# Performance work log

Hardware: AMD Instinct MI355X
Metric: run time of the kernel (lower is better)

Reference implementation:

```python
import jax, jax.numpy as jnp
import numpy as np

N_QUBITS = 8
N_LAYERS = 4


def _apply_1q(state, U, q):
    """Apply a 2x2 gate U (shape (2,2) shared, or (B,2,2) per-sample) on qubit q.
    state: (B, 2, 2, ..., 2) with qubit q on axis q+1 (wire 0 = most significant)."""
    a = q + 1
    st = jnp.moveaxis(state, a, -1)
    shp = st.shape
    st = st.reshape(shp[0], -1, 2)  # (B, rest, 2)
    if U.ndim == 3:
        st = jnp.einsum('bij,brj->bri', U, st)
    else:
        st = jnp.einsum('ij,brj->bri', U, st)
    return jnp.moveaxis(st.reshape(shp), -1, a)


def _cnot(state, c, t):
    ac, at = c + 1, t + 1
    s0 = jnp.take(state, 0, axis=ac)
    s1 = jnp.take(state, 1, axis=ac)
    at2 = at - 1 if at > ac else at  # axis shift after removing control axis
    s1 = jnp.flip(s1, axis=at2)      # X on target where control = 1
    return jnp.stack([s0, s1], axis=ac)


def _rx(t):
    c = jnp.cos(t / 2)
    s = jnp.sin(t / 2)
    return jnp.stack([jnp.stack([c + 0j, -1j * s]),
                      jnp.stack([-1j * s, c + 0j])]).astype(jnp.complex64)


def _ry(t):
    c = jnp.cos(t / 2)
    s = jnp.sin(t / 2)
    return jnp.stack([jnp.stack([c, -s]),
                      jnp.stack([s, c])]).astype(jnp.complex64)


def _rz(t):
    return jnp.diag(jnp.stack([jnp.exp(-1j * t / 2),
                               jnp.exp(1j * t / 2)])).astype(jnp.complex64)


def _ry_batched(t):
    # t: (B,) -> (B, 2, 2)
    c = jnp.cos(t / 2)
    s = jnp.sin(t / 2)
    U = jnp.stack([jnp.stack([c, -s], axis=-1),
                   jnp.stack([s, c], axis=-1)], axis=-2)
    return U.astype(jnp.complex64)


def setup_inputs() -> dict:
    key = jax.random.key(0)
    k1, k2 = jax.random.split(key)
    B = 16384
    x = jax.random.normal(k1, (B, N_QUBITS), dtype=jnp.float32)
    weights = jax.random.normal(k2, (N_QUBITS * N_LAYERS * 3,), dtype=jnp.float32) * 0.1
    return {"x": x, "weights": weights}


def reference(x, weights):
    n, L = N_QUBITS, N_LAYERS
    B = x.shape[0]
    state = jnp.zeros((B,) + (2,) * n, dtype=jnp.complex64)
    state = state.at[(slice(None),) + (0,) * n].set(1.0)

    # angle encoding: per-sample RY on each wire
    for q in range(n):
        state = _apply_1q(state, _ry_batched(x[:, q]), q)

    idx = 0
    for _ in range(L):
        for q in range(n):
            state = _apply_1q(state, _rx(weights[idx]), q)
            state = _apply_1q(state, _ry(weights[idx + 1]), q)
            state = _apply_1q(state, _rz(weights[idx + 2]), q)
            idx += 3
        for q in range(n - 1):
            state = _cnot(state, q, q + 1)

    p = jnp.abs(state) ** 2  # (B, 2, ..., 2) float32
    outs = []
    for q in range(n):
        axes = tuple(a for a in range(1, n + 1) if a != q + 1)
        z = p.sum(axis=axes)  # (B, 2)
        outs.append(z[:, 0] - z[:, 1])
    return jnp.stack(outs, axis=-1).astype(jnp.float32)
```

## Files before the change

kernel.cpp:

```cpp
#include <hip/hip_runtime.h>


#define NGATES 32

constexpr bool selon(int l, int d) {
    return (l == 0) ? (d == 0) : (((d + l - 1) & (l - 1)) == (l - 1));
}
constexpr int lm_of(int l, int q) {
    int m = 0;
    for (int d = 0; q + d <= 7; ++d)
        if ((l & d) == d) { int qq = q + d; if (qq <= 3) m |= 1 << (3 - qq); }
    return m;
}
constexpr int rm_of(int l, int q) {
    int m = 0;
    for (int d = 0; q + d <= 7; ++d)
        if ((l & d) == d) { int qq = q + d; if (qq >= 4) m |= 1 << (7 - qq); }
    return m;
}
constexpr int slm_of(int l, int q) {
    int m = 0;
    for (int d = 0; d <= q; ++d)
        if (selon(l, d)) { int k = q - d; if (k <= 3) m |= 1 << (3 - k); }
    return m;
}
constexpr int srm_of(int l, int q) {
    int m = 0;
    for (int d = 0; d <= q; ++d)
        if (selon(l, d)) { int k = q - d; if (k >= 4) m |= 1 << (7 - k); }
    return m;
}

__device__ __forceinline__ float xsgn(float f, unsigned m) {
    return __int_as_float(__float_as_int(f) ^ (int)m);
}

template<int M>
__device__ __forceinline__ float shx(float v) {
    return __int_as_float(__builtin_amdgcn_ds_swizzle(__float_as_int(v), (M << 10) | 0x1F));
}

template<int LM, int RM, int SLM, int SRM>
__device__ __forceinline__ void apply_gate(float ar[16], float ai[16], int lane,
                                           const float4 g)
{
    unsigned sm = 0;
    if constexpr (SLM != 0)
        sm = (unsigned)((__builtin_popcount(lane & SLM) & 1) << 31);
    const float c0r = g.x, c1i = g.w;
    const float c0i0 = xsgn(g.y, sm);
    const float c1r0 = xsgn(g.z, sm);
    const float c0i1 = xsgn(g.y, sm ^ 0x80000000u);
    const float c1r1 = xsgn(g.z, sm ^ 0x80000000u);

    if constexpr (RM == 0) {
        #pragma unroll
        for (int r = 0; r < 16; ++r) {
            const bool c1 = (__builtin_popcount(r & SRM) & 1) != 0;
            const float c0i = c1 ? c0i1 : c0i0;
            const float c1r = c1 ? c1r1 : c1r0;
            const float br = shx<LM>(ar[r]);
            const float bi = shx<LM>(ai[r]);
            const float nr = c0r*ar[r] - c0i*ai[r] + c1r*br - c1i*bi;
            const float ni = c0r*ai[r] + c0i*ar[r] + c1r*bi + c1i*br;
            ar[r] = nr; ai[r] = ni;
        }
    } else {
        #pragma unroll
        for (int r = 0; r < 16; ++r) {
            const int p = r ^ RM;
            if (p < r) continue;
            float br_r, bi_r, br_p, bi_p;
            if constexpr (LM != 0) {
                br_r = shx<LM>(ar[p]); bi_r = shx<LM>(ai[p]);
                br_p = shx<LM>(ar[r]); bi_p = shx<LM>(ai[r]);
            } else {
                br_r = ar[p]; bi_r = ai[p];
                br_p = ar[r]; bi_p = ai[r];
            }
            const bool cr = (__builtin_popcount(r & SRM) & 1) != 0;
            const bool cp = (__builtin_popcount(p & SRM) & 1) != 0;
            const float c0i_r = cr ? c0i1 : c0i0, c1r_r = cr ? c1r1 : c1r0;
            const float c0i_p = cp ? c0i1 : c0i0, c1r_p = cp ? c1r1 : c1r0;
            const float nr_r = c0r*ar[r] - c0i_r*ai[r] + c1r_r*br_r - c1i*bi_r;
            const float ni_r = c0r*ai[r] + c0i_r*ar[r] + c1r_r*bi_r + c1i*br_r;
            const float nr_p = c0r*ar[p] - c0i_p*ai[p] + c1r_p*br_p - c1i*bi_p;
            const float ni_p = c0r*ai[p] + c0i_p*ar[p] + c1r_p*bi_p + c1i*br_p;
            ar[r] = nr_r; ai[r] = ni_r;
            ar[p] = nr_p; ai[p] = ni_p;
        }
    }
}

#define GATE(L, Q) apply_gate<lm_of(L,Q), rm_of(L,Q), slm_of(L,Q), srm_of(L,Q)>( \
                       ar, ai, lane, gsh4[(L)*8+(Q)])
#define LAYER(L) GATE(L,0); GATE(L,1); GATE(L,2); GATE(L,3); \
                 GATE(L,4); GATE(L,5); GATE(L,6); GATE(L,7);

__global__ __launch_bounds__(256, 4) void qsim(const float* __restrict__ x,
                                               const float* __restrict__ w,
                                               float* __restrict__ out, int B)
{
    __shared__ float4 gsh4[NGATES];

    const int tid = threadIdx.x;
    if (tid < NGATES) {
        float hx = 0.5f * w[tid*3+0];
        float hy = 0.5f * w[tid*3+1];
        float hz = 0.5f * w[tid*3+2];
        float cx = cosf(hx), sx = sinf(hx);
        float cy = cosf(hy), sy = sinf(hy);
        float cz = cosf(hz), sz = sinf(hz);
        float m00r = cy*cx,  m00i =  sy*sx;
        float m01r = -sy*cx, m01i = -cy*sx;
        gsh4[tid] = make_float4(cz*m00r + sz*m00i,
                                cz*m00i - sz*m00r,
                                cz*m01r + sz*m01i,
                                cz*m01i - sz*m01r);
    }
    __syncthreads();

    const int lane = tid & 63;
    const int il   = lane & 15;
    const int sample = blockIdx.x * 16 + (tid >> 4);
    if (sample >= B) return;

    const float4* xp = (const float4*)(x + sample * 8);
    float4 xa = xp[0], xb = xp[1];
    float xs[8] = {xa.x, xa.y, xa.z, xa.w, xb.x, xb.y, xb.z, xb.w};
    float cq[8], sq[8];
    #pragma unroll
    for (int q = 0; q < 8; ++q) {
        float h = 0.5f * xs[q];
        __sincosf(h, &sq[q], &cq[q]);
    }
    float lp = ((il & 8) ? sq[0] : cq[0]);
    lp      *= ((il & 4) ? sq[1] : cq[1]);
    lp      *= ((il & 2) ? sq[2] : cq[2]);
    lp      *= ((il & 1) ? sq[3] : cq[3]);
    float t67[4] = {cq[6]*cq[7], cq[6]*sq[7], sq[6]*cq[7], sq[6]*sq[7]};
    float a5[2]  = {cq[5], sq[5]};
    float a4[2]  = {cq[4]*lp, sq[4]*lp};
    float ar[16], ai[16];
    #pragma unroll
    for (int r = 0; r < 16; ++r) {
        ar[r] = a4[(r >> 3) & 1] * a5[(r >> 2) & 1] * t67[r & 3];
        ai[r] = 0.f;
    }

    LAYER(0)
    LAYER(1)
    LAYER(2)
    LAYER(3)

    float p[16];
    #pragma unroll
    for (int r = 0; r < 16; ++r) p[r] = ar[r]*ar[r] + ai[r]*ai[r];

    float s0[8], d0[8];
    #pragma unroll
    for (int k = 0; k < 8; ++k) { s0[k] = p[2*k] + p[2*k+1]; d0[k] = p[2*k] - p[2*k+1]; }
    float A0 = ((d0[0]+d0[1]) + (d0[2]+d0[3])) + ((d0[4]+d0[5]) + (d0[6]+d0[7]));
    float s1[4], d1[4];
    #pragma unroll
    for (int k = 0; k < 4; ++k) { s1[k] = s0[2*k] + s0[2*k+1]; d1[k] = s0[2*k] - s0[2*k+1]; }
    float A1 = (d1[0]+d1[1]) + (d1[2]+d1[3]);
    float s2[2], d2[2];
    #pragma unroll
    for (int k = 0; k < 2; ++k) { s2[k] = s1[2*k] + s1[2*k+1]; d2[k] = s1[2*k] - s1[2*k+1]; }
    float A2 = d2[0] + d2[1];
    float A3 = s2[0] - s2[1];
    float P  = s2[0] + s2[1];

    const unsigned sg1 = (unsigned)(il & 1) << 31;
    const unsigned sg2 = (unsigned)(il & 2) << 30;
    const unsigned sg4 = (unsigned)(il & 4) << 29;
    const unsigned sg8 = (unsigned)(il & 8) << 28;

    float wP = P;
    { float t = shx<1>(wP); wP = t + xsgn(wP, sg1); }
    { float t = shx<2>(wP); wP = t + xsgn(wP, sg2); }
    { float t = shx<4>(wP); wP = t + xsgn(wP, sg4); }
    { float t = shx<8>(wP); wP = t + xsgn(wP, sg8); }

    float a3 = xsgn(A3, sg8);
    a3 += shx<1>(a3); a3 += shx<2>(a3); a3 += shx<4>(a3); a3 += shx<8>(a3);
    float a2 = xsgn(A2, sg4);
    a2 += shx<1>(a2); a2 += shx<2>(a2); a2 += shx<4>(a2); a2 += shx<8>(a2);
    float a1 = xsgn(A1, sg2);
    a1 += shx<1>(a1); a1 += shx<2>(a1); a1 += shx<4>(a1); a1 += shx<8>(a1);
    float a0 = xsgn(A0, sg1);
    a0 += shx<1>(a0); a0 += shx<2>(a0); a0 += shx<4>(a0); a0 += shx<8>(a0);

    float* op = out + sample * 8;
    if (il == 8)      { op[0] = wP; op[4] = a3; }
    else if (il == 4) { op[1] = wP; op[5] = a2; }
    else if (il == 2) { op[2] = wP; op[6] = a1; }
    else if (il == 1) { op[3] = wP; op[7] = a0; }
}

extern "C" void kernel_launch(void* const* d_in, const int* in_sizes, int n_in,
                              void* d_out, int out_size, void* d_ws, size_t ws_size,
                              hipStream_t stream) {
    const float* x = (const float*)d_in[0];
    const float* w = (const float*)d_in[1];
    float* out = (float*)d_out;
    const int B = in_sizes[0] / 8;
    const int blocks = (B + 15) / 16;
    qsim<<<blocks, 256, 0, stream>>>(x, w, out, B);
}
```

Before: 78.73 us.

## Replace per-sample circuit simulation with shared unitary and bf16 MFMA GEMM

```diff
diff --git a/kernel.cpp b/kernel.cpp
--- a/kernel.cpp
+++ b/kernel.cpp
@@ -2,42 +2,48 @@
 
 
 #define NGATES 32
-
-constexpr bool selon(int l, int d) {
-    return (l == 0) ? (d == 0) : (((d + l - 1) & (l - 1)) == (l - 1));
-}
-constexpr int lm_of(int l, int q) {
-    int m = 0;
-    for (int d = 0; q + d <= 7; ++d)
-        if ((l & d) == d) { int qq = q + d; if (qq <= 3) m |= 1 << (3 - qq); }
-    return m;
-}
-constexpr int rm_of(int l, int q) {
-    int m = 0;
-    for (int d = 0; q + d <= 7; ++d)
-        if ((l & d) == d) { int qq = q + d; if (qq >= 4) m |= 1 << (7 - qq); }
-    return m;
-}
-constexpr int slm_of(int l, int q) {
-    int m = 0;
-    for (int d = 0; d <= q; ++d)
-        if (selon(l, d)) { int k = q - d; if (k <= 3) m |= 1 << (3 - k); }
-    return m;
-}
-constexpr int srm_of(int l, int q) {
-    int m = 0;
-    for (int d = 0; d <= q; ++d)
-        if (selon(l, d)) { int k = q - d; if (k >= 4) m |= 1 << (7 - k); }
-    return m;
-}
-
+typedef short s8v __attribute__((ext_vector_type(8)));
+typedef float f4v __attribute__((ext_vector_type(4)));
+
+__device__ __forceinline__ unsigned short f2bf(float f) {
+    unsigned u = __float_as_uint(f);
+    u += 0x7FFFu + ((u >> 16) & 1u);
+    return (unsigned short)(u >> 16);
+}
 __device__ __forceinline__ float xsgn(float f, unsigned m) {
     return __int_as_float(__float_as_int(f) ^ (int)m);
 }
-
 template<int M>
 __device__ __forceinline__ float shx(float v) {
     return __int_as_float(__builtin_amdgcn_ds_swizzle(__float_as_int(v), (M << 10) | 0x1F));
+}
+
+constexpr bool selon(int l, int d) {
+    return (l == 0) ? (d == 0) : (((d + l - 1) & (l - 1)) == (l - 1));
+}
+constexpr int lm_of(int l, int q) {
+    int m = 0;
+    for (int d = 0; q + d <= 7; ++d)
+        if ((l & d) == d) { int qq = q + d; if (qq <= 3) m |= 1 << (3 - qq); }
+    return m;
+}
+constexpr int rm_of(int l, int q) {
+    int m = 0;
+    for (int d = 0; q + d <= 7; ++d)
+        if ((l & d) == d) { int qq = q + d; if (qq >= 4) m |= 1 << (7 - qq); }
+    return m;
+}
+constexpr int slm_of(int l, int q) {
+    int m = 0;
+    for (int d = 0; d <= q; ++d)
+        if (selon(l, d)) { int k = q - d; if (k <= 3) m |= 1 << (3 - k); }
+    return m;
+}
+constexpr int srm_of(int l, int q) {
+    int m = 0;
+    for (int d = 0; d <= q; ++d)
+        if (selon(l, d)) { int k = q - d; if (k >= 4) m |= 1 << (7 - k); }
+    return m;
 }
 
 template<int LM, int RM, int SLM, int SRM>
@@ -97,12 +103,10 @@
 #define LAYER(L) GATE(L,0); GATE(L,1); GATE(L,2); GATE(L,3); \
                  GATE(L,4); GATE(L,5); GATE(L,6); GATE(L,7);
 
-__global__ __launch_bounds__(256, 4) void qsim(const float* __restrict__ x,
-                                               const float* __restrict__ w,
-                                               float* __restrict__ out, int B)
+__global__ __launch_bounds__(256) void build_w(const float* __restrict__ w,
+                                               unsigned short* __restrict__ W)
 {
     __shared__ float4 gsh4[NGATES];
-
     const int tid = threadIdx.x;
     if (tid < NGATES) {
         float hx = 0.5f * w[tid*3+0];
@@ -122,81 +126,158 @@
 
     const int lane = tid & 63;
     const int il   = lane & 15;
-    const int sample = blockIdx.x * 16 + (tid >> 4);
-    if (sample >= B) return;
-
-    const float4* xp = (const float4*)(x + sample * 8);
-    float4 xa = xp[0], xb = xp[1];
-    float xs[8] = {xa.x, xa.y, xa.z, xa.w, xb.x, xb.y, xb.z, xb.w};
-    float cq[8], sq[8];
-    #pragma unroll
-    for (int q = 0; q < 8; ++q) {
-        float h = 0.5f * xs[q];
-        __sincosf(h, &sq[q], &cq[q]);
-    }
-    float lp = ((il & 8) ? sq[0] : cq[0]);
-    lp      *= ((il & 4) ? sq[1] : cq[1]);
-    lp      *= ((il & 2) ? sq[2] : cq[2]);
-    lp      *= ((il & 1) ? sq[3] : cq[3]);
-    float t67[4] = {cq[6]*cq[7], cq[6]*sq[7], sq[6]*cq[7], sq[6]*sq[7]};
-    float a5[2]  = {cq[5], sq[5]};
-    float a4[2]  = {cq[4]*lp, sq[4]*lp};
+    const int j    = blockIdx.x * 16 + (tid >> 4);
+
     float ar[16], ai[16];
     #pragma unroll
     for (int r = 0; r < 16; ++r) {
-        ar[r] = a4[(r >> 3) & 1] * a5[(r >> 2) & 1] * t67[r & 3];
+        ar[r] = (((j >> 4) == il) && ((j & 15) == r)) ? 1.f : 0.f;
         ai[r] = 0.f;
     }
-
     LAYER(0)
     LAYER(1)
     LAYER(2)
     LAYER(3)
-
-    float p[16];
-    #pragma unroll
-    for (int r = 0; r < 16; ++r) p[r] = ar[r]*ar[r] + ai[r]*ai[r];
-
-    float s0[8], d0[8];
-    #pragma unroll
-    for (int k = 0; k < 8; ++k) { s0[k] = p[2*k] + p[2*k+1]; d0[k] = p[2*k] - p[2*k+1]; }
-    float A0 = ((d0[0]+d0[1]) + (d0[2]+d0[3])) + ((d0[4]+d0[5]) + (d0[6]+d0[7]));
-    float s1[4], d1[4];
-    #pragma unroll
-    for (int k = 0; k < 4; ++k) { s1[k] = s0[2*k] + s0[2*k+1]; d1[k] = s0[2*k] - s0[2*k+1]; }
-    float A1 = (d1[0]+d1[1]) + (d1[2]+d1[3]);
-    float s2[2], d2[2];
-    #pragma unroll
-    for (int k = 0; k < 2; ++k) { s2[k] = s1[2*k] + s1[2*k+1]; d2[k] = s1[2*k] - s1[2*k+1]; }
-    float A2 = d2[0] + d2[1];
-    float A3 = s2[0] - s2[1];
-    float P  = s2[0] + s2[1];
-
-    const unsigned sg1 = (unsigned)(il & 1) << 31;
-    const unsigned sg2 = (unsigned)(il & 2) << 30;
-    const unsigned sg4 = (unsigned)(il & 4) << 29;
-    const unsigned sg8 = (unsigned)(il & 8) << 28;
-
-    float wP = P;
-    { float t = shx<1>(wP); wP = t + xsgn(wP, sg1); }
-    { float t = shx<2>(wP); wP = t + xsgn(wP, sg2); }
-    { float t = shx<4>(wP); wP = t + xsgn(wP, sg4); }
-    { float t = shx<8>(wP); wP = t + xsgn(wP, sg8); }
-
-    float a3 = xsgn(A3, sg8);
-    a3 += shx<1>(a3); a3 += shx<2>(a3); a3 += shx<4>(a3); a3 += shx<8>(a3);
-    float a2 = xsgn(A2, sg4);
-    a2 += shx<1>(a2); a2 += shx<2>(a2); a2 += shx<4>(a2); a2 += shx<8>(a2);
-    float a1 = xsgn(A1, sg2);
-    a1 += shx<1>(a1); a1 += shx<2>(a1); a1 += shx<4>(a1); a1 += shx<8>(a1);
-    float a0 = xsgn(A0, sg1);
-    a0 += shx<1>(a0); a0 += shx<2>(a0); a0 += shx<4>(a0); a0 += shx<8>(a0);
-
-    float* op = out + sample * 8;
-    if (il == 8)      { op[0] = wP; op[4] = a3; }
-    else if (il == 4) { op[1] = wP; op[5] = a2; }
-    else if (il == 2) { op[2] = wP; op[6] = a1; }
-    else if (il == 1) { op[3] = wP; op[7] = a0; }
+    #pragma unroll
+    for (int r = 0; r < 16; ++r) {
+        const int i = (il << 4) | r;
+        W[i * 256 + j]         = f2bf(ar[r]);
+        W[(256 + i) * 256 + j] = f2bf(ai[r]);
+    }
+}
+
+__global__ __launch_bounds__(256, 4) void gemm_z(const float* __restrict__ x,
+                                                 const unsigned short* __restrict__ W,
+                                                 float* __restrict__ out, int B)
+{
+    __shared__ __align__(16) unsigned short El[16 * 264];
+    __shared__ float zbuf[4][16][8];
+
+    const int tid = threadIdx.x;
+    const int Mbase = blockIdx.x * 16;
+
+    {
+        const int s  = tid >> 4;
+        const int tk = tid & 15;
+        const float4* xp = (const float4*)(x + (Mbase + s) * 8);
+        float4 xa = xp[0], xb = xp[1];
+        float xs8[8] = {xa.x, xa.y, xa.z, xa.w, xb.x, xb.y, xb.z, xb.w};
+        float c[8], sn[8];
+        #pragma unroll
+        for (int q = 0; q < 8; ++q) __sincosf(0.5f * xs8[q], &sn[q], &c[q]);
+        float base = ((tk & 8) ? sn[0] : c[0]) * ((tk & 4) ? sn[1] : c[1])
+                   * ((tk & 2) ? sn[2] : c[2]) * ((tk & 1) ? sn[3] : c[3]);
+        float P45[4] = {c[4]*c[5], c[4]*sn[5], sn[4]*c[5], sn[4]*sn[5]};
+        float P67[4] = {c[6]*c[7], c[6]*sn[7], sn[6]*c[7], sn[6]*sn[7]};
+        unsigned short* dst = &El[s * 264 + tk * 16];
+        #pragma unroll
+        for (int v = 0; v < 16; ++v)
+            dst[v] = f2bf(base * P45[v >> 2] * P67[v & 3]);
+    }
+    __syncthreads();
+
+    const int lane = tid & 63;
+    const int g    = tid >> 6;
+    const int col  = lane & 15;
+    const int quad = lane >> 4;
+
+    f4v accR[4], accI[4];
+    #pragma unroll
+    for (int nt = 0; nt < 4; ++nt) {
+        accR[nt] = (f4v){0.f, 0.f, 0.f, 0.f};
+        accI[nt] = (f4v){0.f, 0.f, 0.f, 0.f};
+    }
+
+    const s8v* Wp = (const s8v*)W;
+    const s8v* Ap = (const s8v*)El;
+
+    #pragma unroll
+    for (int ks = 0; ks < 8; ++ks) {
+        const s8v a = Ap[col * 33 + ks * 4 + quad];
+        #pragma unroll
+        for (int nt = 0; nt < 4; ++nt) {
+            const int nR = g * 64 + nt * 16 + col;
+            const s8v bR = Wp[nR * 32 + ks * 4 + quad];
+            accR[nt] = __builtin_amdgcn_mfma_f32_16x16x32_bf16(a, bR, accR[nt], 0, 0, 0);
+            const s8v bI = Wp[(nR + 256) * 32 + ks * 4 + quad];
+            accI[nt] = __builtin_amdgcn_mfma_f32_16x16x32_bf16(a, bI, accI[nt], 0, 0, 0);
+        }
+    }
+
+    float S0[4], S1[4], S2[4];
+    #pragma unroll
+    for (int reg = 0; reg < 4; ++reg) {
+        float p0 = accR[0][reg]*accR[0][reg] + accI[0][reg]*accI[0][reg];
+        float p1 = accR[1][reg]*accR[1][reg] + accI[1][reg]*accI[1][reg];
+        float p2 = accR[2][reg]*accR[2][reg] + accI[2][reg]*accI[2][reg];
+        float p3 = accR[3][reg]*accR[3][reg] + accI[3][reg]*accI[3][reg];
+        S0[reg] = (p0 + p1) + (p2 + p3);
+        S1[reg] = (p0 + p1) - (p2 + p3);
+        S2[reg] = (p0 - p1) + (p2 - p3);
+    }
+
+    const unsigned b1 = (unsigned)(col & 1) << 31;
+    const unsigned b2 = (unsigned)(col & 2) << 30;
+    const unsigned b4 = (unsigned)(col & 4) << 29;
+    const unsigned b8 = (unsigned)(col & 8) << 28;
+    #pragma unroll
+    for (int reg = 0; reg < 4; ++reg) {
+        float v;
+        v = S0[reg];
+        { float t = shx<1>(v); v = t + xsgn(v, b1); }
+        { float t = shx<2>(v); v = t + xsgn(v, b2); }
+        { float t = shx<4>(v); v = t + xsgn(v, b4); }
+        { float t = shx<8>(v); v = t + xsgn(v, b8); }
+        S0[reg] = v;
+        v = S1[reg];
+        { float t = shx<1>(v); v = t + xsgn(v, b1); }
+        { float t = shx<2>(v); v = t + xsgn(v, b2); }
+        { float t = shx<4>(v); v = t + xsgn(v, b4); }
+        { float t = shx<8>(v); v = t + xsgn(v, b8); }
+        S1[reg] = v;
+        v = S2[reg];
+        { float t = shx<1>(v); v = t + xsgn(v, b1); }
+        { float t = shx<2>(v); v = t + xsgn(v, b2); }
+        { float t = shx<4>(v); v = t + xsgn(v, b4); }
+        { float t = shx<8>(v); v = t + xsgn(v, b8); }
+        S2[reg] = v;
+    }
+
+    const unsigned sgG1 = (unsigned)(g & 2) << 30;
+    const unsigned sgG0 = (unsigned)(g & 1) << 31;
+    if (col == 0) {
+        #pragma unroll
+        for (int reg = 0; reg < 4; ++reg) {
+            const int row = quad * 4 + reg;
+            zbuf[g][row][0] = xsgn(S0[reg], sgG1);
+            zbuf[g][row][1] = xsgn(S0[reg], sgG0);
+            zbuf[g][row][2] = S1[reg];
+            zbuf[g][row][3] = S2[reg];
+        }
+    } else if (col == 8) {
+        #pragma unroll
+        for (int reg = 0; reg < 4; ++reg)
+            zbuf[g][quad * 4 + reg][4] = xsgn(S0[reg], sgG1);
+    } else if (col == 4) {
+        #pragma unroll
+        for (int reg = 0; reg < 4; ++reg)
+            zbuf[g][quad * 4 + reg][5] = xsgn(S0[reg], sgG0);
+    } else if (col == 2) {
+        #pragma unroll
+        for (int reg = 0; reg < 4; ++reg)
+            zbuf[g][quad * 4 + reg][6] = S1[reg];
+    } else if (col == 1) {
+        #pragma unroll
+        for (int reg = 0; reg < 4; ++reg)
+            zbuf[g][quad * 4 + reg][7] = S2[reg];
+    }
+    __syncthreads();
+
+    if (tid < 128) {
+        const int row = tid >> 3, q = tid & 7;
+        out[(Mbase + row) * 8 + q] = (zbuf[0][row][q] + zbuf[1][row][q])
+                                   + (zbuf[2][row][q] + zbuf[3][row][q]);
+    }
 }
 
 extern "C" void kernel_launch(void* const* d_in, const int* in_sizes, int n_in,
@@ -205,7 +286,8 @@
     const float* x = (const float*)d_in[0];
     const float* w = (const float*)d_in[1];
     float* out = (float*)d_out;
+    unsigned short* W = (unsigned short*)d_ws;
     const int B = in_sizes[0] / 8;
-    const int blocks = (B + 15) / 16;
-    qsim<<<blocks, 256, 0, stream>>>(x, w, out, B);
-}
+    build_w<<<16, 256, 0, stream>>>(w, W);
+    gemm_z<<<B / 16, 256, 0, stream>>>(x, W, out, B);
+}
```

Measured after the change: 102.0 us. 1.29x slower.
